# Performance work log

Measured on AMD Instinct MI355X. Metric: run time of the kernel, lower is better.

The kernel has to match this reference:

```python
import jax, jax.numpy as jnp
import numpy as np

B, T, F, H = 512, 1024, 64, 128

def setup_inputs() -> dict:
    key = jax.random.key(0)
    ks = jax.random.split(key, 6)
    x = jax.random.normal(ks[0], (B, T, F), dtype=jnp.float32)
    # Keras LSTM params: kernel [F,4H], recurrent_kernel [H,4H], bias [4H]; gate order i,f,g,o
    W = jax.random.normal(ks[1], (F, 4 * H), dtype=jnp.float32) * (1.0 / np.sqrt(F))
    U = jax.random.normal(ks[2], (H, 4 * H), dtype=jnp.float32) * (1.0 / np.sqrt(H))
    b = jnp.zeros((4 * H,), dtype=jnp.float32)
    Wfc = jax.random.normal(ks[3], (H, 1), dtype=jnp.float32) * (1.0 / np.sqrt(H))
    bfc = jnp.zeros((1,), dtype=jnp.float32)
    return {"x": x, "W": W, "U": U, "b": b, "Wfc": Wfc, "bfc": bfc}

def reference(x, W, U, b, Wfc, bfc):
    # LSTM with recurrent_activation='tanh' (gates i,f,o use tanh, NOT sigmoid);
    # candidate g and cell-output activation are also tanh (Keras defaults).
    batch = x.shape[0]
    h0 = jnp.zeros((batch, H), dtype=x.dtype)
    c0 = jnp.zeros((batch, H), dtype=x.dtype)

    def step(carry, xt):
        h, c = carry
        z = xt @ W + h @ U + b  # [B, 4H]
        i, f, g, o = jnp.split(z, 4, axis=-1)
        i = jnp.tanh(i)
        f = jnp.tanh(f)
        g = jnp.tanh(g)
        o = jnp.tanh(o)
        c_new = f * c + i * g
        h_new = o * jnp.tanh(c_new)
        return (h_new, c_new), None

    xs = jnp.swapaxes(x, 0, 1)  # [T, B, F]
    (h_last, _), _ = jax.lax.scan(step, (h0, c0), xs)
    return h_last @ Wfc + bfc  # [B, 1]
```

## Files before the change

### kernel.cpp

```cpp
#include <hip/hip_runtime.h>

typedef _Float16 h8  __attribute__((ext_vector_type(8)));
typedef _Float16 hh4 __attribute__((ext_vector_type(4)));
typedef float    f4  __attribute__((ext_vector_type(4)));

#define TT 1024
#define FF 64
#define NTH 512
#define GRP 16
#define NGRP (TT / GRP)
#define K2 2.8853900817779268f

#define HSWZ(r, e) ((e) ^ (((r) & 7) << 3))

__device__ __forceinline__ float tanh0(float z) {
  float e = __builtin_amdgcn_exp2f(z * K2);
  return __builtin_fmaf(-2.0f, __builtin_amdgcn_rcpf(e + 1.0f), 1.0f);
}

#define MFMA __builtin_amdgcn_mfma_f32_16x16x32_f16

__global__ __launch_bounds__(NTH, 2) void lstm_persist(
    const float* __restrict__ X, const float* __restrict__ W,
    const float* __restrict__ U, const float* __restrict__ bias,
    const float* __restrict__ Wfc, const float* __restrict__ bfcp,
    float* __restrict__ out)
{
  const int tid = threadIdx.x;
  const int wv = tid >> 6, ln = tid & 63;
  const int l15 = ln & 15, lg = ln >> 4;
  const int row0 = blockIdx.x * 2;
  const int ncol = wv * 16 + l15;

  __shared__ __align__(16) _Float16 h_s[2][2 * 128];
  __shared__ __align__(16) _Float16 x_s[32 * 64];
  __shared__ __align__(16) _Float16 zx_s[32 * 512];
  __shared__ float red[8][2];

  h8 uf[4][4], wf4[4][2];
  f4 bias4[4];
#pragma unroll
  for (int g = 0; g < 4; ++g) {
    const int n = g * 128 + ncol;
#pragma unroll
    for (int f = 0; f < 4; ++f) {
      h8 v;
#pragma unroll
      for (int e = 0; e < 8; ++e) v[e] = (_Float16)U[(32 * f + 8 * lg + e) * 512 + n];
      uf[g][f] = v;
    }
#pragma unroll
    for (int f = 0; f < 2; ++f) {
      h8 v;
#pragma unroll
      for (int e = 0; e < 8; ++e) v[e] = (_Float16)W[(32 * f + 8 * lg + e) * 512 + n];
      wf4[g][f] = v;
    }
    const float bv = bias[n];
    f4 b4 = {bv, bv, bv, bv};
    bias4[g] = b4;
  }
  const float wfc = Wfc[ncol];

  int hofs[4];
#pragma unroll
  for (int f = 0; f < 4; ++f) {
    const int base = 32 * f + 8 * lg;
    hofs[f] = (l15 == 0) ? base : (l15 == 4) ? 128 + base : 0;
  }
  int bxofs[2][2];
#pragma unroll
  for (int mt = 0; mt < 2; ++mt)
#pragma unroll
    for (int f = 0; f < 2; ++f)
      bxofs[mt][f] = HSWZ(l15, (mt * 16 + l15) * 64 + 32 * f + 8 * lg);

  const int zofs  = (lg < 2) ? (lg * 512 + ncol * 4) : 0;
  const int zwofs = ncol * 4;
  const int hwofs = (lg & 1) * 128 + ncol;

  const int sm = tid >> 4;
  const int sk = (tid & 15) * 4;
  const int sxofs = HSWZ(sm, sm * 64 + sk);
  const size_t xoff0 = (size_t)(row0 + (sm & 1)) * (TT * FF) + (size_t)(sm >> 1) * FF + sk;

  ((_Float16*)h_s)[tid] = (_Float16)0.0f;

  f4 xg = *(const f4*)(X + xoff0);
  float cc = 0.f;
  const f4 zq = {0.f, 0.f, 0.f, 0.f};
  __syncthreads();

#define STEP(S, CUR, NXT) {                                                   \
    const _Float16* hb = &h_s[CUR][0];                                        \
    h8 ha0 = *(const h8*)(hb + hofs[0]);                                      \
    h8 ha1 = *(const h8*)(hb + hofs[1]);                                      \
    h8 ha2 = *(const h8*)(hb + hofs[2]);                                      \
    h8 ha3 = *(const h8*)(hb + hofs[3]);                                      \
    hh4 q4 = *(const hh4*)(&zx_s[zofs + (S) * 1024]);                         \
    f4 a0 = MFMA(ha0, uf[0][0], zq, 0, 0, 0);                                 \
    f4 a1 = MFMA(ha0, uf[1][0], zq, 0, 0, 0);                                 \
    f4 a2 = MFMA(ha0, uf[2][0], zq, 0, 0, 0);                                 \
    f4 a3 = MFMA(ha0, uf[3][0], zq, 0, 0, 0);                                 \
    a0 = MFMA(ha1, uf[0][1], a0, 0, 0, 0);                                    \
    a1 = MFMA(ha1, uf[1][1], a1, 0, 0, 0);                                    \
    a2 = MFMA(ha1, uf[2][1], a2, 0, 0, 0);                                    \
    a3 = MFMA(ha1, uf[3][1], a3, 0, 0, 0);                                    \
    a0 = MFMA(ha2, uf[0][2], a0, 0, 0, 0);                                    \
    a1 = MFMA(ha2, uf[1][2], a1, 0, 0, 0);                                    \
    a2 = MFMA(ha2, uf[2][2], a2, 0, 0, 0);                                    \
    a3 = MFMA(ha2, uf[3][2], a3, 0, 0, 0);                                    \
    a0 = MFMA(ha3, uf[0][3], a0, 0, 0, 0);                                    \
    a1 = MFMA(ha3, uf[1][3], a1, 0, 0, 0);                                    \
    a2 = MFMA(ha3, uf[2][3], a2, 0, 0, 0);                                    \
    a3 = MFMA(ha3, uf[3][3], a3, 0, 0, 0);                                    \
    float zi = a0[0] + (float)q4[0];                                          \
    float zf = a1[0] + (float)q4[1];                                          \
    float zc = a2[0] + (float)q4[2];                                          \
    float zo = a3[0] + (float)q4[3];                                          \
    float ti = tanh0(zi), tf = tanh0(zf), tg = tanh0(zc), to = tanh0(zo);     \
    cc = __builtin_fmaf(tf, cc, ti * tg);                                     \
    float hv = to * tanh0(cc);                                                \
    if (lg < 2) h_s[NXT][hwofs] = (_Float16)hv;                               \
    __syncthreads();                                                          \
  }

#pragma unroll 1
  for (int grp = 0; grp < NGRP; ++grp) {
    {
      hh4 pk;
#pragma unroll
      for (int j = 0; j < 4; ++j) pk[j] = (_Float16)xg[j];
      *(hh4*)(&x_s[sxofs]) = pk;
    }
    __syncthreads();

    h8 xa00 = *(const h8*)(&x_s[bxofs[0][0]]);
    h8 xa01 = *(const h8*)(&x_s[bxofs[0][1]]);
    h8 xa10 = *(const h8*)(&x_s[bxofs[1][0]]);
    h8 xa11 = *(const h8*)(&x_s[bxofs[1][1]]);
    f4 b00 = MFMA(xa00, wf4[0][0], bias4[0], 0, 0, 0);
    f4 b01 = MFMA(xa00, wf4[1][0], bias4[1], 0, 0, 0);
    f4 b02 = MFMA(xa00, wf4[2][0], bias4[2], 0, 0, 0);
    f4 b03 = MFMA(xa00, wf4[3][0], bias4[3], 0, 0, 0);
    b00 = MFMA(xa01, wf4[0][1], b00, 0, 0, 0);
    b01 = MFMA(xa01, wf4[1][1], b01, 0, 0, 0);
    b02 = MFMA(xa01, wf4[2][1], b02, 0, 0, 0);
    b03 = MFMA(xa01, wf4[3][1], b03, 0, 0, 0);
    f4 b10 = MFMA(xa10, wf4[0][0], bias4[0], 0, 0, 0);
    f4 b11 = MFMA(xa10, wf4[1][0], bias4[1], 0, 0, 0);
    f4 b12 = MFMA(xa10, wf4[2][0], bias4[2], 0, 0, 0);
    f4 b13 = MFMA(xa10, wf4[3][0], bias4[3], 0, 0, 0);
    b10 = MFMA(xa11, wf4[0][1], b10, 0, 0, 0);
    b11 = MFMA(xa11, wf4[1][1], b11, 0, 0, 0);
    b12 = MFMA(xa11, wf4[2][1], b12, 0, 0, 0);
    b13 = MFMA(xa11, wf4[3][1], b13, 0, 0, 0);
#pragma unroll
    for (int j = 0; j < 4; ++j) {
      hh4 p0; p0[0] = (_Float16)b00[j]; p0[1] = (_Float16)b01[j];
              p0[2] = (_Float16)b02[j]; p0[3] = (_Float16)b03[j];
      *(hh4*)(&zx_s[(0 * 16 + 4 * lg + j) * 512 + zwofs]) = p0;
      hh4 p1; p1[0] = (_Float16)b10[j]; p1[1] = (_Float16)b11[j];
              p1[2] = (_Float16)b12[j]; p1[3] = (_Float16)b13[j];
      *(hh4*)(&zx_s[(1 * 16 + 4 * lg + j) * 512 + zwofs]) = p1;
    }
    {
      const int t0n = (grp + 1 < NGRP ? grp + 1 : grp) * GRP;
      xg = *(const f4*)(X + xoff0 + (size_t)t0n * FF);
    }
    __syncthreads();

#pragma unroll
    for (int s2 = 0; s2 < 8; ++s2) {
      STEP(2 * s2,     0, 1)
      STEP(2 * s2 + 1, 1, 0)
    }
  }
#undef STEP

  float hw0 = (float)h_s[0][ncol];
  float hw1 = (float)h_s[0][128 + ncol];
  float p0 = hw0 * wfc;
  float p1 = hw1 * wfc;
#pragma unroll
  for (int m = 1; m < 16; m <<= 1) {
    p0 += __shfl_xor(p0, m, 16);
    p1 += __shfl_xor(p1, m, 16);
  }
  if (ln == 0) { red[wv][0] = p0; red[wv][1] = p1; }
  __syncthreads();
  if (tid < 2) {
    float y = bfcp[0];
#pragma unroll
    for (int w2 = 0; w2 < 8; ++w2) y += red[w2][tid];
    out[row0 + tid] = y;
  }
}

extern "C" void kernel_launch(void* const* d_in, const int* in_sizes, int n_in,
                              void* d_out, int out_size, void* d_ws, size_t ws_size,
                              hipStream_t stream) {
  const float* x   = (const float*)d_in[0];
  const float* W   = (const float*)d_in[1];
  const float* U   = (const float*)d_in[2];
  const float* b   = (const float*)d_in[3];
  const float* Wfc = (const float*)d_in[4];
  const float* bfc = (const float*)d_in[5];
  float* out = (float*)d_out;
  hipLaunchKernelGGL(lstm_persist, dim3(256), dim3(NTH), 0, stream,
                     x, W, U, b, Wfc, bfc, out);
}
```

Baseline: 482.5 us.

## Serialize gate MFMA chains with sched barriers, prefetch input projection, remove store branch

Reorders the recurrent MFMAs so each gate's 4-MFMA chain finishes and its tanh runs before the next gate starts, with scheduling barriers that hold this order so activation math overlaps later MFMAs. The per-step load of the precomputed input projection is moved to the end of the previous step, taking the LDS read off the critical path. The h store is made unconditional by giving the inactive lane groups a dummy region in an enlarged h buffer, which removes the branch. The cost is serialized MFMA dependency chains, which may expose MFMA latency, plus a slightly larger shared buffer.

```diff
diff --git a/kernel.cpp b/kernel.cpp
--- a/kernel.cpp
+++ b/kernel.cpp
@@ -19,6 +19,7 @@
 }
 
 #define MFMA __builtin_amdgcn_mfma_f32_16x16x32_f16
+#define FENCE() __builtin_amdgcn_sched_barrier(0)
 
 __global__ __launch_bounds__(NTH, 2) void lstm_persist(
     const float* __restrict__ X, const float* __restrict__ W,
@@ -32,7 +33,7 @@
   const int row0 = blockIdx.x * 2;
   const int ncol = wv * 16 + l15;
 
-  __shared__ __align__(16) _Float16 h_s[2][2 * 128];
+  __shared__ __align__(16) _Float16 h_s[2][384];
   __shared__ __align__(16) _Float16 x_s[32 * 64];
   __shared__ __align__(16) _Float16 zx_s[32 * 512];
   __shared__ float red[8][2];
@@ -77,51 +78,54 @@
 
   const int zofs  = (lg < 2) ? (lg * 512 + ncol * 4) : 0;
   const int zwofs = ncol * 4;
-  const int hwofs = (lg & 1) * 128 + ncol;
+  const int hwofs = (lg < 2) ? (lg * 128 + ncol) : (256 + ncol);
 
   const int sm = tid >> 4;
   const int sk = (tid & 15) * 4;
   const int sxofs = HSWZ(sm, sm * 64 + sk);
   const size_t xoff0 = (size_t)(row0 + (sm & 1)) * (TT * FF) + (size_t)(sm >> 1) * FF + sk;
 
-  ((_Float16*)h_s)[tid] = (_Float16)0.0f;
+  for (int i = tid; i < 2 * 384; i += NTH) ((_Float16*)h_s)[i] = (_Float16)0.0f;
 
   f4 xg = *(const f4*)(X + xoff0);
   float cc = 0.f;
   const f4 zq = {0.f, 0.f, 0.f, 0.f};
+  hh4 q4cur;
   __syncthreads();
 
-#define STEP(S, CUR, NXT) {                                                   \
+#define STEP(S, CUR, NXT, DOPF) {                                             \
     const _Float16* hb = &h_s[CUR][0];                                        \
     h8 ha0 = *(const h8*)(hb + hofs[0]);                                      \
     h8 ha1 = *(const h8*)(hb + hofs[1]);                                      \
     h8 ha2 = *(const h8*)(hb + hofs[2]);                                      \
     h8 ha3 = *(const h8*)(hb + hofs[3]);                                      \
-    hh4 q4 = *(const hh4*)(&zx_s[zofs + (S) * 1024]);                         \
     f4 a0 = MFMA(ha0, uf[0][0], zq, 0, 0, 0);                                 \
+    a0 = MFMA(ha1, uf[0][1], a0, 0, 0, 0);                                    \
+    a0 = MFMA(ha2, uf[0][2], a0, 0, 0, 0);                                    \
+    a0 = MFMA(ha3, uf[0][3], a0, 0, 0, 0);                                    \
+    float ti = tanh0(a0[0] + (float)q4cur[0]);                                \
+    FENCE();                                                                  \
     f4 a1 = MFMA(ha0, uf[1][0], zq, 0, 0, 0);                                 \
+    a1 = MFMA(ha1, uf[1][1], a1, 0, 0, 0);                                    \
+    a1 = MFMA(ha2, uf[1][2], a1, 0, 0, 0);                                    \
+    a1 = MFMA(ha3, uf[1][3], a1, 0, 0, 0);                                    \
+    float tf = tanh0(a1[0] + (float)q4cur[1]);                                \
+    FENCE();                                                                  \
     f4 a2 = MFMA(ha0, uf[2][0], zq, 0, 0, 0);                                 \
+    a2 = MFMA(ha1, uf[2][1], a2, 0, 0, 0);                                    \
+    a2 = MFMA(ha2, uf[2][2], a2, 0, 0, 0);                                    \
+    a2 = MFMA(ha3, uf[2][3], a2, 0, 0, 0);                                    \
+    float tg = tanh0(a2[0] + (float)q4cur[2]);                                \
+    cc = __builtin_fmaf(tf, cc, ti * tg);                                     \
+    FENCE();                                                                  \
     f4 a3 = MFMA(ha0, uf[3][0], zq, 0, 0, 0);                                 \
-    a0 = MFMA(ha1, uf[0][1], a0, 0, 0, 0);                                    \
-    a1 = MFMA(ha1, uf[1][1], a1, 0, 0, 0);                                    \
-    a2 = MFMA(ha1, uf[2][1], a2, 0, 0, 0);                                    \
     a3 = MFMA(ha1, uf[3][1], a3, 0, 0, 0);                                    \
-    a0 = MFMA(ha2, uf[0][2], a0, 0, 0, 0);                                    \
-    a1 = MFMA(ha2, uf[1][2], a1, 0, 0, 0);                                    \
-    a2 = MFMA(ha2, uf[2][2], a2, 0, 0, 0);                                    \
     a3 = MFMA(ha2, uf[3][2], a3, 0, 0, 0);                                    \
-    a0 = MFMA(ha3, uf[0][3], a0, 0, 0, 0);                                    \
-    a1 = MFMA(ha3, uf[1][3], a1, 0, 0, 0);                                    \
-    a2 = MFMA(ha3, uf[2][3], a2, 0, 0, 0);                                    \
     a3 = MFMA(ha3, uf[3][3], a3, 0, 0, 0);                                    \
-    float zi = a0[0] + (float)q4[0];                                          \
-    float zf = a1[0] + (float)q4[1];                                          \
-    float zc = a2[0] + (float)q4[2];                                          \
-    float zo = a3[0] + (float)q4[3];                                          \
-    float ti = tanh0(zi), tf = tanh0(zf), tg = tanh0(zc), to = tanh0(zo);     \
-    cc = __builtin_fmaf(tf, cc, ti * tg);                                     \
+    float to = tanh0(a3[0] + (float)q4cur[3]);                                \
     float hv = to * tanh0(cc);                                                \
-    if (lg < 2) h_s[NXT][hwofs] = (_Float16)hv;                               \
+    h_s[NXT][hwofs] = (_Float16)hv;                                           \
+    if (DOPF) q4cur = *(const hh4*)(&zx_s[zofs + ((S) + 1) * 1024]);          \
     __syncthreads();                                                          \
   }
 
@@ -169,11 +173,12 @@
       xg = *(const f4*)(X + xoff0 + (size_t)t0n * FF);
     }
     __syncthreads();
+    q4cur = *(const hh4*)(&zx_s[zofs]);
 
 #pragma unroll
     for (int s2 = 0; s2 < 8; ++s2) {
-      STEP(2 * s2,     0, 1)
-      STEP(2 * s2 + 1, 1, 0)
+      STEP(2 * s2,     0, 1, 1)
+      STEP(2 * s2 + 1, 1, 0, (2 * s2 + 1) != (GRP - 1))
     }
   }
 #undef STEP
```

New measurement: 462.3 us. -4.2%, faster.
